# Kernel optimization log

Measured on AMD Instinct MI355X. Metric: run time of the kernel, lower is better.

Reference implementation:

```python
import jax, jax.numpy as jnp
import numpy as np

B = 4
T, Hh, Ww = 16, 32, 32
C = 256
HEADS = 8
WIN = 4
SHIFT = 2
MLP = 1024


def _rel_pos_index(w):
    coords = np.stack(np.meshgrid(np.arange(w), np.arange(w), np.arange(w), indexing='ij')).reshape(3, -1)
    rc = (coords[:, :, None] - coords[:, None, :]).transpose(1, 2, 0)
    rc[:, :, 0] += w - 1
    rc[:, :, 1] += w - 1
    rc[:, :, 2] += w - 1
    rc[:, :, 0] *= (2 * w - 1) * (2 * w - 1)
    rc[:, :, 1] *= 2 * w - 1
    return rc.sum(-1).astype(np.int32)  # (w^3, w^3)


def _attn_mask(t, h, w, win, shift):
    m = np.zeros((t, h, w))
    sl = (slice(0, -win), slice(-win, -shift), slice(-shift, None))
    cnt = 0
    for a in sl:
        for b in sl:
            for c in sl:
                m[a, b, c] = cnt
                cnt += 1
    m = m.reshape(t // win, win, h // win, win, w // win, win).transpose(0, 2, 4, 1, 3, 5).reshape(-1, win ** 3)
    am = m[:, None, :] - m[:, :, None]  # (nW, N, N)
    return np.where(am != 0, -100.0, 0.0).astype(np.float32)


def setup_inputs() -> dict:
    key = jax.random.key(0)
    ks = jax.random.split(key, 12)
    s_in = 1.0 / np.sqrt(C)
    s_mlp = 1.0 / np.sqrt(MLP)
    return {
        'x': jax.random.normal(ks[0], (B, T * Hh * Ww, C), jnp.float32),
        'norm1_g': jnp.ones((C,), jnp.float32),
        'norm1_b': jnp.zeros((C,), jnp.float32),
        'qkv_w': jax.random.normal(ks[1], (C, 3 * C), jnp.float32) * s_in,
        'qkv_b': jax.random.normal(ks[2], (3 * C,), jnp.float32) * 0.02,
        'proj_w': jax.random.normal(ks[3], (C, C), jnp.float32) * s_in,
        'proj_b': jax.random.normal(ks[4], (C,), jnp.float32) * 0.02,
        'rel_bias_table': jax.random.normal(ks[5], ((2 * WIN - 1) ** 3, HEADS), jnp.float32) * 0.02,
        'norm2_g': jnp.ones((C,), jnp.float32),
        'norm2_b': jnp.zeros((C,), jnp.float32),
        'mlp_w1': jax.random.normal(ks[6], (C, MLP), jnp.float32) * s_in,
        'mlp_b1': jax.random.normal(ks[7], (MLP,), jnp.float32) * 0.02,
        'mlp_w2': jax.random.normal(ks[8], (MLP, C), jnp.float32) * s_mlp,
        'mlp_b2': jax.random.normal(ks[9], (C,), jnp.float32) * 0.02,
        'rel_index': jnp.asarray(_rel_pos_index(WIN)),
        'attn_mask': jnp.asarray(_attn_mask(T, Hh, Ww, WIN, SHIFT)),
    }


def _ln(x, g, b, eps):
    mu = x.mean(-1, keepdims=True)
    var = ((x - mu) ** 2).mean(-1, keepdims=True)
    return (x - mu) * jax.lax.rsqrt(var + eps) * g + b


def reference(x, norm1_g, norm1_b, qkv_w, qkv_b, proj_w, proj_b, rel_bias_table,
              norm2_g, norm2_b, mlp_w1, mlp_b1, mlp_w2, mlp_b2, rel_index, attn_mask):
    w = WIN
    N = w ** 3
    hd = C // HEADS
    scale = hd ** -0.5

    h = _ln(x, norm1_g, norm1_b, 1e-5).reshape(B, T, Hh, Ww, C)
    h = jnp.roll(h, shift=(-SHIFT, -SHIFT, -SHIFT), axis=(1, 2, 3))
    # window partition -> (B*nW, N, C)
    h = h.reshape(B, T // w, w, Hh // w, w, Ww // w, w, C)
    h = h.transpose(0, 1, 3, 5, 2, 4, 6, 7).reshape(-1, N, C)

    qkv = (h @ qkv_w + qkv_b).reshape(-1, N, 3, HEADS, hd)
    qkv = qkv.transpose(2, 0, 3, 1, 4)  # (3, BW, heads, N, hd)
    q, k, v = qkv[0] * scale, qkv[1], qkv[2]
    attn = jnp.einsum('bhid,bhjd->bhij', q, k)

    bias = rel_bias_table[rel_index.reshape(-1)].reshape(N, N, HEADS).transpose(2, 0, 1)
    attn = attn + bias[None]

    nW = attn_mask.shape[0]
    attn = attn.reshape(-1, nW, HEADS, N, N) + attn_mask[None, :, None]
    attn = jax.nn.softmax(attn.reshape(-1, HEADS, N, N), axis=-1)

    o = jnp.einsum('bhij,bhjd->bhid', attn, v).transpose(0, 2, 1, 3).reshape(-1, N, C)
    o = o @ proj_w + proj_b
    # window reverse
    o = o.reshape(B, T // w, Hh // w, Ww // w, w, w, w, C)
    o = o.transpose(0, 1, 4, 2, 5, 3, 6, 7).reshape(B, T, Hh, Ww, C)
    o = jnp.roll(o, shift=(SHIFT, SHIFT, SHIFT), axis=(1, 2, 3)).reshape(B, T * Hh * Ww, C)

    x = x + o
    y = _ln(x, norm2_g, norm2_b, 1e-6)
    y = jax.nn.gelu(y @ mlp_w1 + mlp_b1, approximate=False) @ mlp_w2 + mlp_b2
    return x + y
```

## Files before the change

kernel.cpp:

```cpp
#include <hip/hip_runtime.h>
#include <cstdint>
#include <cstddef>

typedef float  f32x4_t  __attribute__((ext_vector_type(4)));
typedef __bf16 bf16x8_t __attribute__((ext_vector_type(8)));
typedef __bf16 bf16x4_t __attribute__((ext_vector_type(4)));

#define NTOK   65536
#define CCH    256
#define NWINT  1024

__device__ __forceinline__ float wred_sum(float v) {
#pragma unroll
  for (int off = 32; off > 0; off >>= 1) v += __shfl_xor(v, off, 64);
  return v;
}

__device__ __forceinline__ void gload16(void* lds, const void* g) {
  __builtin_amdgcn_global_load_lds(
      (const __attribute__((address_space(1))) uint32_t*)g,
      (__attribute__((address_space(3))) uint32_t*)lds, 16, 0, 0);
}

__device__ __forceinline__ int win_to_orig(int token) {
  int gid = token >> 6, n = token & 63;
  int bb = gid >> 8, rem = gid & 255;
  int t = (((rem >> 6) << 2) + (n >> 4) + 2) & 15;
  int h = ((((rem >> 3) & 7) << 2) + ((n >> 2) & 3) + 2) & 31;
  int w = (((rem & 7) << 2) + (n & 3) + 2) & 31;
  return ((bb * 16 + t) * 32 + h) * 32 + w;
}

__device__ __forceinline__ float gelu_f(float v) {
  float u = v * (0.7978845608028654f + 0.03567740814f * v * v);
  float t = 1.0f - 2.0f / (__expf(2.0f * u) + 1.0f);
  return 0.5f * v * (1.0f + t);
}

__global__ __launch_bounds__(256) void prep_weights(
    const float* __restrict__ qkv_w, const float* __restrict__ proj_w,
    const float* __restrict__ mlp_w1, const float* __restrict__ mlp_w2,
    __bf16* __restrict__ wt_qkv, __bf16* __restrict__ wt_proj,
    __bf16* __restrict__ wt_mlp1, __bf16* __restrict__ wt_mlp2) {
  int i = blockIdx.x * 256 + threadIdx.x;
  if (i < 196608) {
    int k = i / 768, n = i % 768;
    wt_qkv[n * 256 + k] = (__bf16)qkv_w[i];
  } else if (i < 262144) {
    int j = i - 196608;
    int k = j >> 8, n = j & 255;
    wt_proj[n * 256 + k] = (__bf16)proj_w[j];
  } else if (i < 524288) {
    int j = i - 262144;
    int k = j >> 10, n = j & 1023;
    wt_mlp1[n * 256 + k] = (__bf16)mlp_w1[j];
  } else {
    int j = i - 524288;
    int k = j >> 8, n = j & 255;
    wt_mlp2[n * 1024 + k] = (__bf16)mlp_w2[j];
  }
}

__global__ __launch_bounds__(256) void cm_prep(
    const float* __restrict__ table, const int* __restrict__ ridx,
    const float* __restrict__ mask, __bf16* __restrict__ cm) {
  int tid = blockIdx.x * 256 + threadIdx.x;
  int l = tid & 63;
  int t16 = (tid >> 6) & 15;
  int h = (tid >> 10) & 7;
  int w = tid >> 13;
  int it = t16 & 3, jt = t16 >> 2;
  int i = it * 16 + (l & 15);
  int jb = jt * 16 + ((l >> 4) << 2);
  const float* mrow = mask + (size_t)w * 4096 + i * 64;
  const int* rrow = ridx + i * 64;
  bf16x4_t o;
#pragma unroll
  for (int r = 0; r < 4; ++r) {
    int j = jb + r;
    o[r] = (__bf16)(table[rrow[j] * 8 + h] + mrow[j]);
  }
  *(bf16x4_t*)(cm + (size_t)tid * 4) = o;
}

__global__ __launch_bounds__(256) void ln_kernel(
    const float* __restrict__ xin, const float* __restrict__ g,
    const float* __restrict__ b, __bf16* __restrict__ out, float eps) {
  int token = blockIdx.x * 4 + (threadIdx.x >> 6);
  int lane = threadIdx.x & 63;
  size_t src = (size_t)win_to_orig(token);
  f32x4_t v = ((const f32x4_t*)(xin + src * CCH))[lane];
  float mu = wred_sum(v[0] + v[1] + v[2] + v[3]) * (1.0f / 256.0f);
  float d0 = v[0] - mu, d1 = v[1] - mu, d2 = v[2] - mu, d3 = v[3] - mu;
  float var = wred_sum(d0 * d0 + d1 * d1 + d2 * d2 + d3 * d3) * (1.0f / 256.0f);
  float rs = rsqrtf(var + eps);
  f32x4_t gg = ((const f32x4_t*)g)[lane];
  f32x4_t bb = ((const f32x4_t*)b)[lane];
  bf16x4_t o;
  o[0] = (__bf16)(d0 * rs * gg[0] + bb[0]);
  o[1] = (__bf16)(d1 * rs * gg[1] + bb[1]);
  o[2] = (__bf16)(d2 * rs * gg[2] + bb[2]);
  o[3] = (__bf16)(d3 * rs * gg[3] + bb[3]);
  *(bf16x4_t*)(out + (size_t)token * CCH + lane * 4) = o;
}

#define BMG 128
#define BNG 256
#define BKG 64
__global__ __launch_bounds__(512, 4) void gemm_qkv(
    const __bf16* __restrict__ A, const __bf16* __restrict__ Bt,
    const float* __restrict__ bias, __bf16* __restrict__ outp,
    int N, int K) {
  __shared__ __bf16 smA[BMG * BKG];
  __shared__ __bf16 smB[BNG * BKG];
  const int wv = threadIdx.x >> 6;
  const int ln = threadIdx.x & 63;
  const int i15 = ln & 15, g = ln >> 4;

  int nwg = gridDim.x;
  int wgid = ((int)blockIdx.x & 7) * (nwg >> 3) + ((int)blockIdx.x >> 3);
  int nx = N >> 8;
  int bx = wgid % nx, by = wgid / nx;
  const int bm = by * BMG, bn = bx * BNG;
  const int wr = wv >> 2, wc = wv & 3;

  const __bf16* aP[2];
  const __bf16* bP[4];
#pragma unroll
  for (int it = 0; it < 2; ++it) {
    int slot = (it * 8 + wv) * 64 + ln;
    int row = slot >> 3, chunk = (slot & 7) ^ (row & 7);
    aP[it] = A + (size_t)(bm + row) * K + chunk * 8;
  }
#pragma unroll
  for (int it = 0; it < 4; ++it) {
    int slot = (it * 8 + wv) * 64 + ln;
    int row = slot >> 3, chunk = (slot & 7) ^ (row & 7);
    bP[it] = Bt + (size_t)(bn + row) * K + chunk * 8;
  }

  f32x4_t acc[4][4];
#pragma unroll
  for (int nn = 0; nn < 4; ++nn)
#pragma unroll
    for (int mm = 0; mm < 4; ++mm) acc[nn][mm] = (f32x4_t){0.f, 0.f, 0.f, 0.f};

  const int KT = K >> 6;
  for (int kt = 0; kt < KT; ++kt) {
#pragma unroll
    for (int it = 0; it < 2; ++it) {
      gload16(&smA[(it * 8 + wv) * 512], aP[it]);
      aP[it] += BKG;
    }
#pragma unroll
    for (int it = 0; it < 4; ++it) {
      gload16(&smB[(it * 8 + wv) * 512], bP[it]);
      bP[it] += BKG;
    }
    asm volatile("s_waitcnt vmcnt(0)" ::: "memory");
    __syncthreads();

#pragma unroll
    for (int kh = 0; kh < 2; ++kh) {
      int co = ((kh * 4 + g) ^ (i15 & 7)) * 16;
      bf16x8_t af[4], bfr[4];
#pragma unroll
      for (int mm = 0; mm < 4; ++mm)
        af[mm] = *(const bf16x8_t*)((const char*)smA +
                                    (wr * 64 + mm * 16 + i15) * 128 + co);
#pragma unroll
      for (int nn = 0; nn < 4; ++nn)
        bfr[nn] = *(const bf16x8_t*)((const char*)smB +
                                     (wc * 64 + nn * 16 + i15) * 128 + co);
#pragma unroll
      for (int nn = 0; nn < 4; ++nn)
#pragma unroll
        for (int mm = 0; mm < 4; ++mm)
          acc[nn][mm] = __builtin_amdgcn_mfma_f32_16x16x32_bf16(
              bfr[nn], af[mm], acc[nn][mm], 0, 0, 0);
    }
    __syncthreads();
  }

#pragma unroll
  for (int nn = 0; nn < 4; ++nn) {
    int colg = bn + wc * 64 + nn * 16 + g * 4;
    f32x4_t bv = *(const f32x4_t*)(bias + colg);
#pragma unroll
    for (int mm = 0; mm < 4; ++mm) {
      int rowg = bm + wr * 64 + mm * 16 + i15;
      bf16x4_t o;
#pragma unroll
      for (int r = 0; r < 4; ++r) o[r] = (__bf16)(acc[nn][mm][r] + bv[r]);
      *(bf16x4_t*)(outp + (size_t)rowg * N + colg) = o;
    }
  }
}

__global__ __launch_bounds__(512, 2) void proj_ln(
    const __bf16* __restrict__ A, const __bf16* __restrict__ Bt,
    const float* __restrict__ bias, const float* __restrict__ res,
    const float* __restrict__ g2, const float* __restrict__ b2,
    float* __restrict__ x2, __bf16* __restrict__ yb) {
  __shared__ __bf16 smA[BMG * BKG];
  __shared__ __bf16 smB[BNG * BKG];
  const int wv = threadIdx.x >> 6;
  const int ln = threadIdx.x & 63;
  const int i15 = ln & 15, g = ln >> 4;

  int nwg = gridDim.x;
  int wgid = ((int)blockIdx.x & 7) * (nwg >> 3) + ((int)blockIdx.x >> 3);
  const int bm = wgid * BMG;
  const int wr = wv >> 2, wc = wv & 3;
  const int K = 256;

  const __bf16* aP[2];
  const __bf16* bP[4];
#pragma unroll
  for (int it = 0; it < 2; ++it) {
    int slot = (it * 8 + wv) * 64 + ln;
    int row = slot >> 3, chunk = (slot & 7) ^ (row & 7);
    aP[it] = A + (size_t)(bm + row) * K + chunk * 8;
  }
#pragma unroll
  for (int it = 0; it < 4; ++it) {
    int slot = (it * 8 + wv) * 64 + ln;
    int row = slot >> 3, chunk = (slot & 7) ^ (row & 7);
    bP[it] = Bt + (size_t)row * K + chunk * 8;
  }

  f32x4_t acc[4][4];
#pragma unroll
  for (int nn = 0; nn < 4; ++nn)
#pragma unroll
    for (int mm = 0; mm < 4; ++mm) acc[nn][mm] = (f32x4_t){0.f, 0.f, 0.f, 0.f};

  for (int kt = 0; kt < 4; ++kt) {
#pragma unroll
    for (int it = 0; it < 2; ++it) {
      gload16(&smA[(it * 8 + wv) * 512], aP[it]);
      aP[it] += BKG;
    }
#pragma unroll
    for (int it = 0; it < 4; ++it) {
      gload16(&smB[(it * 8 + wv) * 512], bP[it]);
      bP[it] += BKG;
    }
    asm volatile("s_waitcnt vmcnt(0)" ::: "memory");
    __syncthreads();
#pragma unroll
    for (int kh = 0; kh < 2; ++kh) {
      int co = ((kh * 4 + g) ^ (i15 & 7)) * 16;
      bf16x8_t af[4], bfr[4];
#pragma unroll
      for (int mm = 0; mm < 4; ++mm)
        af[mm] = *(const bf16x8_t*)((const char*)smA +
                                    (wr * 64 + mm * 16 + i15) * 128 + co);
#pragma unroll
      for (int nn = 0; nn < 4; ++nn)
        bfr[nn] = *(const bf16x8_t*)((const char*)smB +
                                     (wc * 64 + nn * 16 + i15) * 128 + co);
#pragma unroll
      for (int nn = 0; nn < 4; ++nn)
#pragma unroll
        for (int mm = 0; mm < 4; ++mm)
          acc[nn][mm] = __builtin_amdgcn_mfma_f32_16x16x32_bf16(
              bfr[nn], af[mm], acc[nn][mm], 0, 0, 0);
    }
    __syncthreads();
  }

  size_t dst[4];
#pragma unroll
  for (int mm = 0; mm < 4; ++mm) {
    int rowg = bm + wr * 64 + mm * 16 + i15;
    dst[mm] = (size_t)win_to_orig(rowg) * CCH;
  }
#pragma unroll
  for (int nn = 0; nn < 4; ++nn) {
    int colg = wc * 64 + nn * 16 + g * 4;
    f32x4_t bv = *(const f32x4_t*)(bias + colg);
#pragma unroll
    for (int mm = 0; mm < 4; ++mm) {
      f32x4_t rv = *(const f32x4_t*)(res + dst[mm] + colg);
#pragma unroll
      for (int r = 0; r < 4; ++r) acc[nn][mm][r] += bv[r] + rv[r];
    }
  }

  float2* stf = (float2*)smA;
#pragma unroll
  for (int mm = 0; mm < 4; ++mm) {
    float s1 = 0.f, s2 = 0.f;
#pragma unroll
    for (int nn = 0; nn < 4; ++nn)
#pragma unroll
      for (int r = 0; r < 4; ++r) {
        float v = acc[nn][mm][r];
        s1 += v;
        s2 += v * v;
      }
    s1 += __shfl_xor(s1, 16, 64);
    s1 += __shfl_xor(s1, 32, 64);
    s2 += __shfl_xor(s2, 16, 64);
    s2 += __shfl_xor(s2, 32, 64);
    if (g == 0) stf[(wr * 64 + mm * 16 + i15) * 4 + wc] = make_float2(s1, s2);
  }
  __syncthreads();
  float mu[4], rs[4];
#pragma unroll
  for (int mm = 0; mm < 4; ++mm) {
    int row = wr * 64 + mm * 16 + i15;
    float S1 = 0.f, S2 = 0.f;
#pragma unroll
    for (int w = 0; w < 4; ++w) {
      float2 p = stf[row * 4 + w];
      S1 += p.x;
      S2 += p.y;
    }
    mu[mm] = S1 * (1.0f / 256.0f);
    rs[mm] = rsqrtf(S2 * (1.0f / 256.0f) - mu[mm] * mu[mm] + 1e-6f);
  }

#pragma unroll
  for (int nn = 0; nn < 4; ++nn) {
    int colg = wc * 64 + nn * 16 + g * 4;
    f32x4_t gv = *(const f32x4_t*)(g2 + colg);
    f32x4_t bv = *(const f32x4_t*)(b2 + colg);
#pragma unroll
    for (int mm = 0; mm < 4; ++mm) {
      f32x4_t v = acc[nn][mm];
      *(f32x4_t*)(x2 + dst[mm] + colg) = v;
      bf16x4_t yo;
#pragma unroll
      for (int r = 0; r < 4; ++r)
        yo[r] = (__bf16)((v[r] - mu[mm]) * rs[mm] * gv[r] + bv[r]);
      *(bf16x4_t*)(yb + dst[mm] + colg) = yo;
    }
  }
}

__global__ __launch_bounds__(256, 2) void mlp_fused(
    const __bf16* __restrict__ yb, const __bf16* __restrict__ w1t,
    const float* __restrict__ b1, const __bf16* __restrict__ w2t,
    const float* __restrict__ b2, float* __restrict__ io) {
  __shared__ __bf16 smA[64 * 64];
  __shared__ __bf16 smW[256 * 64];
  __shared__ __bf16 h1b[64 * 256];
  const int wv = threadIdx.x >> 6;
  const int ln = threadIdx.x & 63;
  const int i15 = ln & 15, g = ln >> 4, wc = wv;

  int nwg = gridDim.x;
  int wgid = ((int)blockIdx.x & 7) * (nwg >> 3) + ((int)blockIdx.x >> 3);
  const int bm = wgid * 64;

  uint32_t aOff[2], w1o[8], w2o[8];
#pragma unroll
  for (int rnd = 0; rnd < 2; ++rnd) {
    int slot = rnd * 256 + (int)threadIdx.x;
    int row = slot >> 3, ch = (slot & 7) ^ (row & 7);
    aOff[rnd] = (uint32_t)((bm + row) * 256 + ch * 8);
  }
#pragma unroll
  for (int rnd = 0; rnd < 8; ++rnd) {
    int slot = rnd * 256 + (int)threadIdx.x;
    int row = slot >> 3, ch = (slot & 7) ^ (row & 7);
    w1o[rnd] = (uint32_t)(row * 256 + ch * 8);
    w2o[rnd] = (uint32_t)(row * 1024 + ch * 8);
  }

  f32x4_t acc2[4][4];
#pragma unroll
  for (int nn = 0; nn < 4; ++nn)
#pragma unroll
    for (int mm = 0; mm < 4; ++mm) acc2[nn][mm] = (f32x4_t){0.f, 0.f, 0.f, 0.f};

  for (int nc = 0; nc < 4; ++nc) {
    f32x4_t acc1[4][4];
#pragma unroll
    for (int nn = 0; nn < 4; ++nn)
#pragma unroll
      for (int mm = 0; mm < 4; ++mm)
        acc1[nn][mm] = (f32x4_t){0.f, 0.f, 0.f, 0.f};

    for (int kt = 0; kt < 4; ++kt) {
#pragma unroll
      for (int rnd = 0; rnd < 2; ++rnd)
        gload16(&smA[(rnd * 4 + wv) * 512], yb + aOff[rnd] + kt * 64);
#pragma unroll
      for (int rnd = 0; rnd < 8; ++rnd)
        gload16(&smW[(rnd * 4 + wv) * 512],
                w1t + nc * 65536 + w1o[rnd] + kt * 64);
      asm volatile("s_waitcnt vmcnt(0)" ::: "memory");
      __syncthreads();
#pragma unroll
      for (int kh = 0; kh < 2; ++kh) {
        int co = ((kh * 4 + g) ^ (i15 & 7)) * 16;
        bf16x8_t af[4], wf[4];
#pragma unroll
        for (int mm = 0; mm < 4; ++mm)
          af[mm] = *(const bf16x8_t*)((const char*)smA +
                                      (mm * 16 + i15) * 128 + co);
#pragma unroll
        for (int nn = 0; nn < 4; ++nn)
          wf[nn] = *(const bf16x8_t*)((const char*)smW +
                                      (wc * 64 + nn * 16 + i15) * 128 + co);
#pragma unroll
        for (int nn = 0; nn < 4; ++nn)
#pragma unroll
          for (int mm = 0; mm < 4; ++mm)
            acc1[nn][mm] = __builtin_amdgcn_mfma_f32_16x16x32_bf16(
                wf[nn], af[mm], acc1[nn][mm], 0, 0, 0);
      }
      __syncthreads();
    }

#pragma unroll
    for (int rnd = 0; rnd < 8; ++rnd)
      gload16(&smW[(rnd * 4 + wv) * 512], w2t + w2o[rnd] + nc * 256);

    const float* b1g = b1 + nc * 256 + wc * 64;
#pragma unroll
    for (int nn = 0; nn < 4; ++nn) {
      f32x4_t bb = *(const f32x4_t*)(b1g + nn * 16 + g * 4);
#pragma unroll
      for (int mm = 0; mm < 4; ++mm) {
        bf16x4_t p;
#pragma unroll
        for (int r = 0; r < 4; ++r)
          p[r] = (__bf16)gelu_f(acc1[nn][mm][r] + bb[r]);
        uint32_t byte =
            (uint32_t)((mm * 16 + i15) * 512 +
                       ((wc * 128 + nn * 32 + g * 8) ^ ((i15 & 7) << 4)));
        *(bf16x4_t*)((char*)h1b + byte) = p;
      }
    }

    for (int kt2 = 0; kt2 < 4; ++kt2) {
      asm volatile("s_waitcnt vmcnt(0)" ::: "memory");
      __syncthreads();
#pragma unroll
      for (int kh = 0; kh < 2; ++kh) {
        int coW = ((kh * 4 + g) ^ (i15 & 7)) * 16;
        int coA = kt2 * 128 + ((kh * 64 + g * 16) ^ ((i15 & 7) << 4));
        bf16x8_t af[4], wf[4];
#pragma unroll
        for (int mm = 0; mm < 4; ++mm)
          af[mm] = *(const bf16x8_t*)((const char*)h1b +
                                      (mm * 16 + i15) * 512 + coA);
#pragma unroll
        for (int nn = 0; nn < 4; ++nn)
          wf[nn] = *(const bf16x8_t*)((const char*)smW +
                                      (wc * 64 + nn * 16 + i15) * 128 + coW);
#pragma unroll
        for (int nn = 0; nn < 4; ++nn)
#pragma unroll
          for (int mm = 0; mm < 4; ++mm)
            acc2[nn][mm] = __builtin_amdgcn_mfma_f32_16x16x32_bf16(
                wf[nn], af[mm], acc2[nn][mm], 0, 0, 0);
      }
      __syncthreads();
      if (kt2 < 3) {
#pragma unroll
        for (int rnd = 0; rnd < 8; ++rnd)
          gload16(&smW[(rnd * 4 + wv) * 512],
                  w2t + w2o[rnd] + nc * 256 + (kt2 + 1) * 64);
      }
    }
  }

#pragma unroll
  for (int nn = 0; nn < 4; ++nn) {
    int colg = wc * 64 + nn * 16 + g * 4;
    f32x4_t bb = *(const f32x4_t*)(b2 + colg);
#pragma unroll
    for (int mm = 0; mm < 4; ++mm) {
      int rowg = bm + mm * 16 + i15;
      float* p = io + (size_t)rowg * 256 + colg;
      f32x4_t rv = *(const f32x4_t*)p;
      f32x4_t o;
#pragma unroll
      for (int r = 0; r < 4; ++r) o[r] = rv[r] + acc2[nn][mm][r] + bb[r];
      *(f32x4_t*)p = o;
    }
  }
}

__global__ __launch_bounds__(256) void attn_mfma(
    const __bf16* __restrict__ qkv, const __bf16* __restrict__ cm,
    __bf16* __restrict__ owin) {
  __shared__ __align__(16) __bf16 smP[4][64 * 72];
  __shared__ __align__(16) __bf16 smV[4][64 * 32];
  const int wv = threadIdx.x >> 6;
  const int ln = threadIdx.x & 63;
  const int task = blockIdx.x * 4 + wv;
  const int win = task >> 3;
  const int h = task & 7;
  const int i15 = ln & 15, g = ln >> 4;

  const __bf16* base = qkv + (size_t)win * 64 * 768 + h * 32;

  {
    __bf16* vdst = smV[wv];
#pragma unroll
    for (int c = 0; c < 4; ++c) {
      const __bf16* src =
          base + (size_t)(c * 16 + (ln >> 2)) * 768 + 512 + (ln & 3) * 8;
      gload16(vdst + c * 512, src);
    }
  }

  bf16x8_t kf[4], qf[4];
#pragma unroll
  for (int t = 0; t < 4; ++t) {
    kf[t] = *(const bf16x8_t*)(base + (size_t)(t * 16 + i15) * 768 + 256 + g * 8);
    qf[t] = *(const bf16x8_t*)(base + (size_t)(t * 16 + i15) * 768 + g * 8);
  }

  f32x4_t st[4][4];
#pragma unroll
  for (int jt = 0; jt < 4; ++jt)
#pragma unroll
    for (int it = 0; it < 4; ++it)
      st[jt][it] = __builtin_amdgcn_mfma_f32_16x16x32_bf16(
          kf[jt], qf[it], (f32x4_t){0.f, 0.f, 0.f, 0.f}, 0, 0, 0);

  const __bf16* cmp = cm + (((size_t)(win & 255) * 8 + h) * 16) * 256;
#pragma unroll
  for (int jt = 0; jt < 4; ++jt)
#pragma unroll
    for (int it = 0; it < 4; ++it) {
      bf16x4_t c4 = *(const bf16x4_t*)(cmp + ((jt * 4 + it) * 64 + ln) * 4);
#pragma unroll
      for (int r = 0; r < 4; ++r)
        st[jt][it][r] =
            fmaf(st[jt][it][r], 0.17677669529663687f, (float)c4[r]);
    }

#pragma unroll
  for (int it = 0; it < 4; ++it) {
    float mx = -1e30f;
#pragma unroll
    for (int jt = 0; jt < 4; ++jt)
#pragma unroll
      for (int r = 0; r < 4; ++r) mx = fmaxf(mx, st[jt][it][r]);
    mx = fmaxf(mx, __shfl_xor(mx, 16, 64));
    mx = fmaxf(mx, __shfl_xor(mx, 32, 64));
    float sum = 0.f;
#pragma unroll
    for (int jt = 0; jt < 4; ++jt)
#pragma unroll
      for (int r = 0; r < 4; ++r) {
        float p = __expf(st[jt][it][r] - mx);
        st[jt][it][r] = p;
        sum += p;
      }
    sum += __shfl_xor(sum, 16, 64);
    sum += __shfl_xor(sum, 32, 64);
    float inv = 1.0f / sum;
#pragma unroll
    for (int jt = 0; jt < 4; ++jt) {
      bf16x4_t p4;
#pragma unroll
      for (int r = 0; r < 4; ++r) p4[r] = (__bf16)(st[jt][it][r] * inv);
      *(bf16x4_t*)(smP[wv] + (it * 16 + i15) * 72 + jt * 16 + g * 4) = p4;
    }
  }
  __syncthreads();

  f32x4_t oacc[4][2];
#pragma unroll
  for (int it = 0; it < 4; ++it)
#pragma unroll
    for (int dt = 0; dt < 2; ++dt) oacc[it][dt] = (f32x4_t){0.f, 0.f, 0.f, 0.f};

  const __bf16* pl = smP[wv];
  const __bf16* vl = smV[wv];
#pragma unroll
  for (int kt = 0; kt < 2; ++kt) {
    bf16x8_t vf[2];
#pragma unroll
    for (int dt = 0; dt < 2; ++dt)
#pragma unroll
      for (int e = 0; e < 8; ++e)
        vf[dt][e] = vl[(kt * 32 + g * 8 + e) * 32 + dt * 16 + i15];
#pragma unroll
    for (int it = 0; it < 4; ++it) {
      bf16x8_t pa =
          *(const bf16x8_t*)(pl + (it * 16 + i15) * 72 + kt * 32 + g * 8);
#pragma unroll
      for (int dt = 0; dt < 2; ++dt)
        oacc[it][dt] = __builtin_amdgcn_mfma_f32_16x16x32_bf16(
            pa, vf[dt], oacc[it][dt], 0, 0, 0);
    }
  }

  __bf16* op = owin + (size_t)win * 64 * 256 + h * 32;
#pragma unroll
  for (int it = 0; it < 4; ++it)
#pragma unroll
    for (int r = 0; r < 4; ++r) {
      int i = it * 16 + g * 4 + r;
#pragma unroll
      for (int dt = 0; dt < 2; ++dt)
        op[(size_t)i * 256 + dt * 16 + i15] = (__bf16)oacc[it][dt][r];
    }
}

extern "C" void kernel_launch(void* const* d_in, const int* in_sizes, int n_in,
                              void* d_out, int out_size, void* d_ws,
                              size_t ws_size, hipStream_t stream) {
  (void)in_sizes; (void)n_in; (void)out_size; (void)ws_size;
  const float* x      = (const float*)d_in[0];
  const float* n1g    = (const float*)d_in[1];
  const float* n1b    = (const float*)d_in[2];
  const float* qkv_w  = (const float*)d_in[3];
  const float* qkv_b  = (const float*)d_in[4];
  const float* proj_w = (const float*)d_in[5];
  const float* proj_b = (const float*)d_in[6];
  const float* rbt    = (const float*)d_in[7];
  const float* n2g    = (const float*)d_in[8];
  const float* n2b    = (const float*)d_in[9];
  const float* mlp_w1 = (const float*)d_in[10];
  const float* mlp_b1 = (const float*)d_in[11];
  const float* mlp_w2 = (const float*)d_in[12];
  const float* mlp_b2 = (const float*)d_in[13];
  const int*   ridx   = (const int*)d_in[14];
  const float* amask  = (const float*)d_in[15];

  char* ws = (char*)d_ws;
  size_t off = 0;
  auto alloc = [&](size_t bytes) {
    void* p = ws + off;
    off += (bytes + 255) & ~(size_t)255;
    return p;
  };
  __bf16* wt_qkv  = (__bf16*)alloc(768 * 256 * 2);
  __bf16* wt_proj = (__bf16*)alloc(256 * 256 * 2);
  __bf16* wt_mlp1 = (__bf16*)alloc(1024 * 256 * 2);
  __bf16* wt_mlp2 = (__bf16*)alloc(1024 * 256 * 2);
  __bf16* hwin = (__bf16*)alloc((size_t)NTOK * 256 * 2);
  __bf16* qkv  = (__bf16*)alloc((size_t)NTOK * 768 * 2);
  __bf16* owin = (__bf16*)alloc((size_t)NTOK * 256 * 2);
  __bf16* cmb  = hwin;
  __bf16* yb   = hwin;
  float* x2    = (float*)d_out;

  prep_weights<<<3072, 256, 0, stream>>>(qkv_w, proj_w, mlp_w1, mlp_w2,
                                         wt_qkv, wt_proj, wt_mlp1, wt_mlp2);
  ln_kernel<<<NTOK / 4, 256, 0, stream>>>(x, n1g, n1b, hwin, 1e-5f);
  gemm_qkv<<<3 * (NTOK / BMG), 512, 0, stream>>>(hwin, wt_qkv, qkv_b, qkv,
                                                 768, 256);
  cm_prep<<<8192, 256, 0, stream>>>(rbt, ridx, amask, cmb);
  attn_mfma<<<2048, 256, 0, stream>>>(qkv, cmb, owin);
  proj_ln<<<NTOK / BMG, 512, 0, stream>>>(owin, wt_proj, proj_b, x, n2g, n2b,
                                          x2, yb);
  mlp_fused<<<NTOK / 64, 256, 0, stream>>>(yb, wt_mlp1, mlp_b1, wt_mlp2,
                                           mlp_b2, x2);
}
```

Measured before the change: 317.2 us.

## Load GEMM operands directly from global into registers instead of LDS staging

Three GEMM kernels (qkv, proj_ln, mlp_fused) stop staging A and weight tiles through LDS with global_load_lds and barriers. Each wave now loads its MFMA fragments straight from global memory into registers, double-buffered across K steps. This removes LDS traffic and per-tile syncs and frees shared memory, but every wave re-reads overlapping operand rows from global/L2 and the loads are less coalesced. The qkv launch bound also drops from 4 to 2 blocks per CU.

```diff
diff --git a/kernel.cpp b/kernel.cpp
--- a/kernel.cpp
+++ b/kernel.cpp
@@ -104,15 +104,16 @@
   *(bf16x4_t*)(out + (size_t)token * CCH + lane * 4) = o;
 }
 
-#define BMG 128
-#define BNG 256
-#define BKG 64
-__global__ __launch_bounds__(512, 4) void gemm_qkv(
+
+#define MFMA16(ACC, W, Af)                                              \
+  _Pragma("unroll") for (int nn = 0; nn < 4; ++nn)                      \
+      _Pragma("unroll") for (int mm = 0; mm < 4; ++mm)                  \
+          ACC[nn][mm] = __builtin_amdgcn_mfma_f32_16x16x32_bf16(        \
+              W[nn], Af[mm], ACC[nn][mm], 0, 0, 0);
+
+__global__ __launch_bounds__(512, 2) void gemm_qkv(
     const __bf16* __restrict__ A, const __bf16* __restrict__ Bt,
-    const float* __restrict__ bias, __bf16* __restrict__ outp,
-    int N, int K) {
-  __shared__ __bf16 smA[BMG * BKG];
-  __shared__ __bf16 smB[BNG * BKG];
+    const float* __restrict__ bias, __bf16* __restrict__ outp, int N) {
   const int wv = threadIdx.x >> 6;
   const int ln = threadIdx.x & 63;
   const int i15 = ln & 15, g = ln >> 4;
@@ -121,22 +122,15 @@
   int wgid = ((int)blockIdx.x & 7) * (nwg >> 3) + ((int)blockIdx.x >> 3);
   int nx = N >> 8;
   int bx = wgid % nx, by = wgid / nx;
-  const int bm = by * BMG, bn = bx * BNG;
+  const int bm = by * 128, bn = bx * 256;
   const int wr = wv >> 2, wc = wv & 3;
 
-  const __bf16* aP[2];
-  const __bf16* bP[4];
-#pragma unroll
-  for (int it = 0; it < 2; ++it) {
-    int slot = (it * 8 + wv) * 64 + ln;
-    int row = slot >> 3, chunk = (slot & 7) ^ (row & 7);
-    aP[it] = A + (size_t)(bm + row) * K + chunk * 8;
-  }
-#pragma unroll
-  for (int it = 0; it < 4; ++it) {
-    int slot = (it * 8 + wv) * 64 + ln;
-    int row = slot >> 3, chunk = (slot & 7) ^ (row & 7);
-    bP[it] = Bt + (size_t)(bn + row) * K + chunk * 8;
+  const __bf16* aP[4];
+  const __bf16* wP[4];
+#pragma unroll
+  for (int q = 0; q < 4; ++q) {
+    aP[q] = A + (size_t)(bm + wr * 64 + q * 16 + i15) * 256 + g * 8;
+    wP[q] = Bt + (size_t)(bn + wc * 64 + q * 16 + i15) * 256 + g * 8;
   }
 
   f32x4_t acc[4][4];
@@ -145,41 +139,28 @@
 #pragma unroll
     for (int mm = 0; mm < 4; ++mm) acc[nn][mm] = (f32x4_t){0.f, 0.f, 0.f, 0.f};
 
-  const int KT = K >> 6;
-  for (int kt = 0; kt < KT; ++kt) {
-#pragma unroll
-    for (int it = 0; it < 2; ++it) {
-      gload16(&smA[(it * 8 + wv) * 512], aP[it]);
-      aP[it] += BKG;
-    }
-#pragma unroll
-    for (int it = 0; it < 4; ++it) {
-      gload16(&smB[(it * 8 + wv) * 512], bP[it]);
-      bP[it] += BKG;
-    }
-    asm volatile("s_waitcnt vmcnt(0)" ::: "memory");
-    __syncthreads();
-
-#pragma unroll
-    for (int kh = 0; kh < 2; ++kh) {
-      int co = ((kh * 4 + g) ^ (i15 & 7)) * 16;
-      bf16x8_t af[4], bfr[4];
-#pragma unroll
-      for (int mm = 0; mm < 4; ++mm)
-        af[mm] = *(const bf16x8_t*)((const char*)smA +
-                                    (wr * 64 + mm * 16 + i15) * 128 + co);
-#pragma unroll
-      for (int nn = 0; nn < 4; ++nn)
-        bfr[nn] = *(const bf16x8_t*)((const char*)smB +
-                                     (wc * 64 + nn * 16 + i15) * 128 + co);
-#pragma unroll
-      for (int nn = 0; nn < 4; ++nn)
-#pragma unroll
-        for (int mm = 0; mm < 4; ++mm)
-          acc[nn][mm] = __builtin_amdgcn_mfma_f32_16x16x32_bf16(
-              bfr[nn], af[mm], acc[nn][mm], 0, 0, 0);
-    }
-    __syncthreads();
+  bf16x8_t a0[4], a1[4], w0[4], w1[4];
+#pragma unroll
+  for (int q = 0; q < 4; ++q) {
+    a0[q] = *(const bf16x8_t*)(aP[q]);
+    w0[q] = *(const bf16x8_t*)(wP[q]);
+  }
+#pragma unroll
+  for (int ks = 0; ks < 8; ks += 2) {
+#pragma unroll
+    for (int q = 0; q < 4; ++q) {
+      a1[q] = *(const bf16x8_t*)(aP[q] + (ks + 1) * 32);
+      w1[q] = *(const bf16x8_t*)(wP[q] + (ks + 1) * 32);
+    }
+    MFMA16(acc, w0, a0);
+    if (ks + 2 < 8) {
+#pragma unroll
+      for (int q = 0; q < 4; ++q) {
+        a0[q] = *(const bf16x8_t*)(aP[q] + (ks + 2) * 32);
+        w0[q] = *(const bf16x8_t*)(wP[q] + (ks + 2) * 32);
+      }
+    }
+    MFMA16(acc, w1, a1);
   }
 
 #pragma unroll
@@ -202,31 +183,22 @@
     const float* __restrict__ bias, const float* __restrict__ res,
     const float* __restrict__ g2, const float* __restrict__ b2,
     float* __restrict__ x2, __bf16* __restrict__ yb) {
-  __shared__ __bf16 smA[BMG * BKG];
-  __shared__ __bf16 smB[BNG * BKG];
+  __shared__ float2 stf[512];
   const int wv = threadIdx.x >> 6;
   const int ln = threadIdx.x & 63;
   const int i15 = ln & 15, g = ln >> 4;
 
   int nwg = gridDim.x;
   int wgid = ((int)blockIdx.x & 7) * (nwg >> 3) + ((int)blockIdx.x >> 3);
-  const int bm = wgid * BMG;
+  const int bm = wgid * 128;
   const int wr = wv >> 2, wc = wv & 3;
-  const int K = 256;
-
-  const __bf16* aP[2];
-  const __bf16* bP[4];
-#pragma unroll
-  for (int it = 0; it < 2; ++it) {
-    int slot = (it * 8 + wv) * 64 + ln;
-    int row = slot >> 3, chunk = (slot & 7) ^ (row & 7);
-    aP[it] = A + (size_t)(bm + row) * K + chunk * 8;
-  }
-#pragma unroll
-  for (int it = 0; it < 4; ++it) {
-    int slot = (it * 8 + wv) * 64 + ln;
-    int row = slot >> 3, chunk = (slot & 7) ^ (row & 7);
-    bP[it] = Bt + (size_t)row * K + chunk * 8;
+
+  const __bf16* aP[4];
+  const __bf16* wP[4];
+#pragma unroll
+  for (int q = 0; q < 4; ++q) {
+    aP[q] = A + (size_t)(bm + wr * 64 + q * 16 + i15) * 256 + g * 8;
+    wP[q] = Bt + (size_t)(wc * 64 + q * 16 + i15) * 256 + g * 8;
   }
 
   f32x4_t acc[4][4];
@@ -235,39 +207,28 @@
 #pragma unroll
     for (int mm = 0; mm < 4; ++mm) acc[nn][mm] = (f32x4_t){0.f, 0.f, 0.f, 0.f};
 
-  for (int kt = 0; kt < 4; ++kt) {
-#pragma unroll
-    for (int it = 0; it < 2; ++it) {
-      gload16(&smA[(it * 8 + wv) * 512], aP[it]);
-      aP[it] += BKG;
-    }
-#pragma unroll
-    for (int it = 0; it < 4; ++it) {
-      gload16(&smB[(it * 8 + wv) * 512], bP[it]);
-      bP[it] += BKG;
-    }
-    asm volatile("s_waitcnt vmcnt(0)" ::: "memory");
-    __syncthreads();
-#pragma unroll
-    for (int kh = 0; kh < 2; ++kh) {
-      int co = ((kh * 4 + g) ^ (i15 & 7)) * 16;
-      bf16x8_t af[4], bfr[4];
-#pragma unroll
-      for (int mm = 0; mm < 4; ++mm)
-        af[mm] = *(const bf16x8_t*)((const char*)smA +
-                                    (wr * 64 + mm * 16 + i15) * 128 + co);
-#pragma unroll
-      for (int nn = 0; nn < 4; ++nn)
-        bfr[nn] = *(const bf16x8_t*)((const char*)smB +
-                                     (wc * 64 + nn * 16 + i15) * 128 + co);
-#pragma unroll
-      for (int nn = 0; nn < 4; ++nn)
-#pragma unroll
-        for (int mm = 0; mm < 4; ++mm)
-          acc[nn][mm] = __builtin_amdgcn_mfma_f32_16x16x32_bf16(
-              bfr[nn], af[mm], acc[nn][mm], 0, 0, 0);
-    }
-    __syncthreads();
+  bf16x8_t a0[4], a1[4], w0[4], w1[4];
+#pragma unroll
+  for (int q = 0; q < 4; ++q) {
+    a0[q] = *(const bf16x8_t*)(aP[q]);
+    w0[q] = *(const bf16x8_t*)(wP[q]);
+  }
+#pragma unroll
+  for (int ks = 0; ks < 8; ks += 2) {
+#pragma unroll
+    for (int q = 0; q < 4; ++q) {
+      a1[q] = *(const bf16x8_t*)(aP[q] + (ks + 1) * 32);
+      w1[q] = *(const bf16x8_t*)(wP[q] + (ks + 1) * 32);
+    }
+    MFMA16(acc, w0, a0);
+    if (ks + 2 < 8) {
+#pragma unroll
+      for (int q = 0; q < 4; ++q) {
+        a0[q] = *(const bf16x8_t*)(aP[q] + (ks + 2) * 32);
+        w0[q] = *(const bf16x8_t*)(wP[q] + (ks + 2) * 32);
+      }
+    }
+    MFMA16(acc, w1, a1);
   }
 
   size_t dst[4];
@@ -288,7 +249,6 @@
     }
   }
 
-  float2* stf = (float2*)smA;
 #pragma unroll
   for (int mm = 0; mm < 4; ++mm) {
     float s1 = 0.f, s2 = 0.f;
@@ -344,30 +304,26 @@
     const __bf16* __restrict__ yb, const __bf16* __restrict__ w1t,
     const float* __restrict__ b1, const __bf16* __restrict__ w2t,
     const float* __restrict__ b2, float* __restrict__ io) {
-  __shared__ __bf16 smA[64 * 64];
-  __shared__ __bf16 smW[256 * 64];
   __shared__ __bf16 h1b[64 * 256];
   const int wv = threadIdx.x >> 6;
   const int ln = threadIdx.x & 63;
   const int i15 = ln & 15, g = ln >> 4, wc = wv;
+  const int sw = (i15 & 7) << 4;
 
   int nwg = gridDim.x;
   int wgid = ((int)blockIdx.x & 7) * (nwg >> 3) + ((int)blockIdx.x >> 3);
   const int bm = wgid * 64;
 
-  uint32_t aOff[2], w1o[8], w2o[8];
-#pragma unroll
-  for (int rnd = 0; rnd < 2; ++rnd) {
-    int slot = rnd * 256 + (int)threadIdx.x;
-    int row = slot >> 3, ch = (slot & 7) ^ (row & 7);
-    aOff[rnd] = (uint32_t)((bm + row) * 256 + ch * 8);
-  }
-#pragma unroll
-  for (int rnd = 0; rnd < 8; ++rnd) {
-    int slot = rnd * 256 + (int)threadIdx.x;
-    int row = slot >> 3, ch = (slot & 7) ^ (row & 7);
-    w1o[rnd] = (uint32_t)(row * 256 + ch * 8);
-    w2o[rnd] = (uint32_t)(row * 1024 + ch * 8);
+  const __bf16* aP[4];
+  const __bf16* w1P[4];
+  const __bf16* w2P[4];
+  int rowoff[4];
+#pragma unroll
+  for (int q = 0; q < 4; ++q) {
+    aP[q] = yb + (size_t)(bm + q * 16 + i15) * 256 + g * 8;
+    w1P[q] = w1t + (size_t)(wc * 64 + q * 16 + i15) * 256 + g * 8;
+    w2P[q] = w2t + (size_t)(wc * 64 + q * 16 + i15) * 1024 + g * 8;
+    rowoff[q] = (q * 16 + i15) * 512;
   }
 
   f32x4_t acc2[4][4];
@@ -376,6 +332,7 @@
 #pragma unroll
     for (int mm = 0; mm < 4; ++mm) acc2[nn][mm] = (f32x4_t){0.f, 0.f, 0.f, 0.f};
 
+#pragma unroll
   for (int nc = 0; nc < 4; ++nc) {
     f32x4_t acc1[4][4];
 #pragma unroll
@@ -384,41 +341,34 @@
       for (int mm = 0; mm < 4; ++mm)
         acc1[nn][mm] = (f32x4_t){0.f, 0.f, 0.f, 0.f};
 
-    for (int kt = 0; kt < 4; ++kt) {
-#pragma unroll
-      for (int rnd = 0; rnd < 2; ++rnd)
-        gload16(&smA[(rnd * 4 + wv) * 512], yb + aOff[rnd] + kt * 64);
-#pragma unroll
-      for (int rnd = 0; rnd < 8; ++rnd)
-        gload16(&smW[(rnd * 4 + wv) * 512],
-                w1t + nc * 65536 + w1o[rnd] + kt * 64);
-      asm volatile("s_waitcnt vmcnt(0)" ::: "memory");
-      __syncthreads();
-#pragma unroll
-      for (int kh = 0; kh < 2; ++kh) {
-        int co = ((kh * 4 + g) ^ (i15 & 7)) * 16;
-        bf16x8_t af[4], wf[4];
-#pragma unroll
-        for (int mm = 0; mm < 4; ++mm)
-          af[mm] = *(const bf16x8_t*)((const char*)smA +
-                                      (mm * 16 + i15) * 128 + co);
-#pragma unroll
-        for (int nn = 0; nn < 4; ++nn)
-          wf[nn] = *(const bf16x8_t*)((const char*)smW +
-                                      (wc * 64 + nn * 16 + i15) * 128 + co);
-#pragma unroll
-        for (int nn = 0; nn < 4; ++nn)
-#pragma unroll
-          for (int mm = 0; mm < 4; ++mm)
-            acc1[nn][mm] = __builtin_amdgcn_mfma_f32_16x16x32_bf16(
-                wf[nn], af[mm], acc1[nn][mm], 0, 0, 0);
-      }
-      __syncthreads();
-    }
-
-#pragma unroll
-    for (int rnd = 0; rnd < 8; ++rnd)
-      gload16(&smW[(rnd * 4 + wv) * 512], w2t + w2o[rnd] + nc * 256);
+    {
+      const __bf16* w1c[4];
+#pragma unroll
+      for (int q = 0; q < 4; ++q) w1c[q] = w1P[q] + nc * 65536;
+      bf16x8_t a0[4], a1[4], w0[4], w1f[4];
+#pragma unroll
+      for (int q = 0; q < 4; ++q) {
+        a0[q] = *(const bf16x8_t*)(aP[q]);
+        w0[q] = *(const bf16x8_t*)(w1c[q]);
+      }
+#pragma unroll
+      for (int ks = 0; ks < 8; ks += 2) {
+#pragma unroll
+        for (int q = 0; q < 4; ++q) {
+          a1[q] = *(const bf16x8_t*)(aP[q] + (ks + 1) * 32);
+          w1f[q] = *(const bf16x8_t*)(w1c[q] + (ks + 1) * 32);
+        }
+        MFMA16(acc1, w0, a0);
+        if (ks + 2 < 8) {
+#pragma unroll
+          for (int q = 0; q < 4; ++q) {
+            a0[q] = *(const bf16x8_t*)(aP[q] + (ks + 2) * 32);
+            w0[q] = *(const bf16x8_t*)(w1c[q] + (ks + 2) * 32);
+          }
+        }
+        MFMA16(acc1, w1f, a1);
+      }
+    }
 
     const float* b1g = b1 + nc * 256 + wc * 64;
 #pragma unroll
@@ -430,44 +380,41 @@
 #pragma unroll
         for (int r = 0; r < 4; ++r)
           p[r] = (__bf16)gelu_f(acc1[nn][mm][r] + bb[r]);
-        uint32_t byte =
-            (uint32_t)((mm * 16 + i15) * 512 +
-                       ((wc * 128 + nn * 32 + g * 8) ^ ((i15 & 7) << 4)));
-        *(bf16x4_t*)((char*)h1b + byte) = p;
-      }
-    }
-
-    for (int kt2 = 0; kt2 < 4; ++kt2) {
-      asm volatile("s_waitcnt vmcnt(0)" ::: "memory");
-      __syncthreads();
-#pragma unroll
-      for (int kh = 0; kh < 2; ++kh) {
-        int coW = ((kh * 4 + g) ^ (i15 & 7)) * 16;
-        int coA = kt2 * 128 + ((kh * 64 + g * 16) ^ ((i15 & 7) << 4));
-        bf16x8_t af[4], wf[4];
-#pragma unroll
-        for (int mm = 0; mm < 4; ++mm)
-          af[mm] = *(const bf16x8_t*)((const char*)h1b +
-                                      (mm * 16 + i15) * 512 + coA);
-#pragma unroll
-        for (int nn = 0; nn < 4; ++nn)
-          wf[nn] = *(const bf16x8_t*)((const char*)smW +
-                                      (wc * 64 + nn * 16 + i15) * 128 + coW);
-#pragma unroll
-        for (int nn = 0; nn < 4; ++nn)
-#pragma unroll
-          for (int mm = 0; mm < 4; ++mm)
-            acc2[nn][mm] = __builtin_amdgcn_mfma_f32_16x16x32_bf16(
-                wf[nn], af[mm], acc2[nn][mm], 0, 0, 0);
-      }
-      __syncthreads();
-      if (kt2 < 3) {
-#pragma unroll
-        for (int rnd = 0; rnd < 8; ++rnd)
-          gload16(&smW[(rnd * 4 + wv) * 512],
-                  w2t + w2o[rnd] + nc * 256 + (kt2 + 1) * 64);
-      }
-    }
+        *(bf16x4_t*)((char*)h1b + rowoff[mm] +
+                     ((wc * 128 + nn * 32 + g * 8) ^ sw)) = p;
+      }
+    }
+    __syncthreads();
+
+    {
+      bf16x8_t h0[4], h1f[4], w0[4], w1f[4];
+#pragma unroll
+      for (int q = 0; q < 4; ++q) {
+        h0[q] = *(const bf16x8_t*)((const char*)h1b + rowoff[q] +
+                                   ((g * 16) ^ sw));
+        w0[q] = *(const bf16x8_t*)(w2P[q] + nc * 256);
+      }
+#pragma unroll
+      for (int ks = 0; ks < 8; ks += 2) {
+#pragma unroll
+        for (int q = 0; q < 4; ++q) {
+          h1f[q] = *(const bf16x8_t*)((const char*)h1b + rowoff[q] +
+                                      (((ks + 1) * 64 + g * 16) ^ sw));
+          w1f[q] = *(const bf16x8_t*)(w2P[q] + nc * 256 + (ks + 1) * 32);
+        }
+        MFMA16(acc2, w0, h0);
+        if (ks + 2 < 8) {
+#pragma unroll
+          for (int q = 0; q < 4; ++q) {
+            h0[q] = *(const bf16x8_t*)((const char*)h1b + rowoff[q] +
+                                       (((ks + 2) * 64 + g * 16) ^ sw));
+            w0[q] = *(const bf16x8_t*)(w2P[q] + nc * 256 + (ks + 2) * 32);
+          }
+        }
+        MFMA16(acc2, w1f, h1f);
+      }
+    }
+    __syncthreads();
   }
 
 #pragma unroll
@@ -650,11 +597,10 @@
   prep_weights<<<3072, 256, 0, stream>>>(qkv_w, proj_w, mlp_w1, mlp_w2,
                                          wt_qkv, wt_proj, wt_mlp1, wt_mlp2);
   ln_kernel<<<NTOK / 4, 256, 0, stream>>>(x, n1g, n1b, hwin, 1e-5f);
-  gemm_qkv<<<3 * (NTOK / BMG), 512, 0, stream>>>(hwin, wt_qkv, qkv_b, qkv,
-                                                 768, 256);
+  gemm_qkv<<<3 * (NTOK / 128), 512, 0, stream>>>(hwin, wt_qkv, qkv_b, qkv, 768);
   cm_prep<<<8192, 256, 0, stream>>>(rbt, ridx, amask, cmb);
   attn_mfma<<<2048, 256, 0, stream>>>(qkv, cmb, owin);
-  proj_ln<<<NTOK / BMG, 512, 0, stream>>>(owin, wt_proj, proj_b, x, n2g, n2b,
+  proj_ln<<<NTOK / 128, 512, 0, stream>>>(owin, wt_proj, proj_b, x, n2g, n2b,
                                           x2, yb);
   mlp_fused<<<NTOK / 64, 256, 0, stream>>>(yb, wt_mlp1, mlp_b1, wt_mlp2,
                                            mlp_b2, x2);
```

After: 456.2 us. 1.44x slower.
